# Kernel tuning notes

Measured on AMD Instinct MI355X. Metric: run time of the kernel, lower is better.

Reference implementation:

```python
import jax, jax.numpy as jnp
import numpy as np

B, T, DIM, H = 2, 2048, 1024, 16
HD = DIM // H  # head_dim = 64
ROPE_BASE = 10000.0


def setup_inputs() -> dict:
    key = jax.random.key(0)
    k1, k2, k3, k4 = jax.random.split(key, 4)
    s = 1.0 / np.sqrt(DIM)
    return {
        "x": jax.random.normal(k1, (B, T, DIM), dtype=jnp.float32),
        "Wqkv": jax.random.normal(k2, (DIM, 3 * DIM), dtype=jnp.float32) * s,
        "Wout": jax.random.normal(k3, (DIM, DIM), dtype=jnp.float32) * s,
        "bout": jax.random.normal(k4, (DIM,), dtype=jnp.float32) * 0.01,
    }


def _rotate_half(x):
    # interleaved rotation: (x0,x1,x2,x3,...) -> (-x1,x0,-x3,x2,...)
    x1 = x[..., ::2]
    x2 = x[..., 1::2]
    return jnp.stack((-x2, x1), axis=-1).reshape(x.shape)


def _rope_cos_sin(seq_len, dtype):
    inv_freq = 1.0 / (ROPE_BASE ** (jnp.arange(0, HD, 2, dtype=jnp.float32) / HD))
    t = jnp.arange(seq_len, dtype=jnp.float32)
    freqs = t[:, None] * inv_freq[None, :]          # [T, HD/2]
    emb = jnp.concatenate((freqs, freqs), axis=-1)  # [T, HD] (cat layout, as in source)
    return jnp.cos(emb).astype(dtype), jnp.sin(emb).astype(dtype)


def reference(x, Wqkv, Wout, bout):
    b, t, _ = x.shape
    qkv = x @ Wqkv                                  # [B, T, 3*DIM]
    q, k, v = jnp.split(qkv, 3, axis=-1)
    # b t (h d) -> b h t d
    reshape = lambda z: z.reshape(b, t, H, HD).transpose(0, 2, 1, 3)
    q, k, v = reshape(q), reshape(k), reshape(v)
    cos, sin = _rope_cos_sin(t, x.dtype)            # [T, HD]
    q = q * cos + _rotate_half(q) * sin
    k = k * cos + _rotate_half(k) * sin
    scale = HD ** -0.5
    scores = jnp.einsum("bhqd,bhkd->bhqk", q, k) * scale
    attn = jax.nn.softmax(scores, axis=-1)
    out = jnp.einsum("bhqk,bhkd->bhqd", attn, v)    # [B, H, T, HD]
    out = out.transpose(0, 2, 1, 3).reshape(b, t, DIM)
    return out @ Wout + bout
```

## Files before the change

kernel.cpp:

```cpp
#include <hip/hip_runtime.h>
#include <math.h>


typedef unsigned short u16;
typedef __attribute__((ext_vector_type(8))) short short8;
typedef __attribute__((ext_vector_type(4))) short short4v;
typedef __attribute__((ext_vector_type(4))) float f32x4;
typedef __attribute__((ext_vector_type(16))) float f32x16;

#define T_SEQ 2048

#if __has_builtin(__builtin_amdgcn_exp2f)
#define EXP2(x) __builtin_amdgcn_exp2f(x)
#else
#define EXP2(x) exp2f(x)
#endif

__device__ __forceinline__ float b2f(u16 u) {
    union { unsigned int i; float f; } x; x.i = ((unsigned int)u) << 16; return x.f;
}
__device__ __forceinline__ u16 f2b(float f) {
    union { float f; unsigned int i; } x; x.f = f;
    return (u16)((x.i + 0x7FFFu + ((x.i >> 16) & 1u)) >> 16);
}
__device__ __forceinline__ void gl_lds16(const u16* g, u16* l) {
    __builtin_amdgcn_global_load_lds(
        (const __attribute__((address_space(1))) unsigned int*)g,
        (__attribute__((address_space(3))) unsigned int*)l, 16, 0, 0);
}
__device__ __forceinline__ short4v pack4(float a, float b, float c, float d) {
    union { float f; unsigned int u; } xa, xb, xc, xd;
    xa.f = a; xb.f = b; xc.f = c; xd.f = d;
    union { unsigned int u2[2]; short4v s; } r;
    r.u2[0] = (xa.u >> 16) | (xb.u & 0xffff0000u);
    r.u2[1] = (xc.u >> 16) | (xd.u & 0xffff0000u);
    return r.s;
}

__global__ __launch_bounds__(256) void setup_kernel(
    const float* __restrict__ x, const float* __restrict__ Wqkv,
    const float* __restrict__ Wout, u16* __restrict__ xb,
    u16* __restrict__ WqkvT, u16* __restrict__ WoutT,
    float* __restrict__ costab, float* __restrict__ sintab)
{
    const int bid = blockIdx.x;
    const int tid = threadIdx.x;

    if (bid < 4096) {
        int i = (bid * 256 + tid) * 4;
        float4 v = *(const float4*)(x + i);
        ushort4 w;
        w.x = f2b(v.x); w.y = f2b(v.y); w.z = f2b(v.z); w.w = f2b(v.w);
        *(ushort4*)(xb + i) = w;
        return;
    }
    if (bid < 8192) {
        const float* in; u16* out; int R, Cn, bx, by;
        if (bid < 7168) { in = Wqkv; out = WqkvT; R = 1024; Cn = 3072;
                          int id = bid - 4096; bx = id % 96; by = id / 96; }
        else            { in = Wout; out = WoutT; R = 1024; Cn = 1024;
                          int id = bid - 7168; bx = id & 31; by = id >> 5; }
        __shared__ u16 tile[32][33];
        const int tx = tid & 31, ty = tid >> 5;
        const int r0 = by * 32, c0 = bx * 32;
#pragma unroll
        for (int rr = ty; rr < 32; rr += 8)
            tile[tx][rr] = f2b(in[(size_t)(r0 + rr) * Cn + c0 + tx]);
        __syncthreads();
#pragma unroll
        for (int rr = ty; rr < 32; rr += 8)
            out[(size_t)(c0 + rr) * R + r0 + tx] = tile[rr][tx];
        return;
    }
    {
        int idx = (bid - 8192) * 256 + tid;
        int t = idx >> 6, d = idx & 63;
        const float nl32 = -0.28782313662425576f;
        float f = __expf((float)(d & 31) * nl32);
        float s, c;
        __sincosf((float)t * f, &s, &c);
        costab[idx] = c; sintab[idx] = s;
    }
}

template<int OBF>
__global__ __launch_bounds__(256) void gemm_bt_mfma(
    const u16* __restrict__ A, const u16* __restrict__ Bt,
    void* __restrict__ Cv, const float* __restrict__ bias,
    int M, int N, int K)
{
    __shared__ u16 As[128 * 32];
    __shared__ u16 Bs[128 * 32];

    const int tid = threadIdx.x;
    const int wave = tid >> 6, lane = tid & 63;
    const int col = lane & 15, quad = lane >> 4;
    const int wm = (wave & 1) * 64, wn = (wave >> 1) * 64;
    const int m0 = blockIdx.y * 128, n0 = blockIdx.x * 128;

    f32x4 acc[4][4];
#pragma unroll
    for (int i = 0; i < 4; ++i)
#pragma unroll
        for (int j = 0; j < 4; ++j) acc[i][j] = f32x4{0.f, 0.f, 0.f, 0.f};

    const int c1 = tid, c2 = tid + 256;
    const u16* a1 = A + (size_t)(m0 + (c1 >> 2)) * K + (c1 & 3) * 8;
    const u16* a2 = A + (size_t)(m0 + (c2 >> 2)) * K + (c2 & 3) * 8;
    const u16* b1 = Bt + (size_t)(n0 + (c1 >> 2)) * K + (c1 & 3) * 8;
    const u16* b2 = Bt + (size_t)(n0 + (c2 >> 2)) * K + (c2 & 3) * 8;
    u16* la1 = As + c1 * 8; u16* la2 = As + c2 * 8;
    u16* lb1 = Bs + c1 * 8; u16* lb2 = Bs + c2 * 8;

    for (int k0 = 0; k0 < K; k0 += 32) {
        __syncthreads();
        gl_lds16(a1 + k0, la1);
        gl_lds16(a2 + k0, la2);
        gl_lds16(b1 + k0, lb1);
        gl_lds16(b2 + k0, lb2);
        __syncthreads();

        short8 af[4], bfr[4];
#pragma unroll
        for (int i = 0; i < 4; ++i) {
            af[i]  = *(const short8*)&As[(wm + i * 16 + col) * 32 + quad * 8];
            bfr[i] = *(const short8*)&Bs[(wn + i * 16 + col) * 32 + quad * 8];
        }
#pragma unroll
        for (int i = 0; i < 4; ++i)
#pragma unroll
            for (int j = 0; j < 4; ++j)
                acc[i][j] = __builtin_amdgcn_mfma_f32_16x16x32_bf16(
                    af[i], bfr[j], acc[i][j], 0, 0, 0);
    }

#pragma unroll
    for (int j = 0; j < 4; ++j) {
        int n = n0 + wn + j * 16 + col;
        float bv = bias ? bias[n] : 0.f;
#pragma unroll
        for (int i = 0; i < 4; ++i) {
            int mbase = m0 + wm + i * 16 + quad * 4;
#pragma unroll
            for (int r = 0; r < 4; ++r) {
                if (OBF) ((u16*)Cv)[(size_t)(mbase + r) * N + n] = f2b(acc[i][j][r] + bv);
                else     ((float*)Cv)[(size_t)(mbase + r) * N + n] = acc[i][j][r] + bv;
            }
        }
    }
}

__global__ __launch_bounds__(256) void prep_kernel(
    const u16* __restrict__ qkvb, const float* __restrict__ costab,
    const float* __restrict__ sintab, u16* __restrict__ Qb,
    u16* __restrict__ Kb, u16* __restrict__ Vimg)
{
    __shared__ u16 Vls[64][72];

    const int tid = threadIdx.x;
    const int bh = blockIdx.y;
    const int t0 = blockIdx.x * 64;
    const int b = bh >> 4, h = bh & 15;
    const int t_loc = tid >> 2;
    const int d0 = (tid & 3) * 16;

    const int t = t0 + t_loc;
    const u16* qp = qkvb + ((size_t)(b * T_SEQ + t)) * 3072 + h * 64 + d0;

    float ct[16], st[16];
    {
        const float* cp = costab + (size_t)t * 64 + d0;
        const float* sp = sintab + (size_t)t * 64 + d0;
#pragma unroll
        for (int j = 0; j < 16; j += 4) {
            *(float4*)&ct[j] = *(const float4*)(cp + j);
            *(float4*)&st[j] = *(const float4*)(sp + j);
        }
    }

#pragma unroll
    for (int part = 0; part < 2; ++part) {
        const float sc = part ? 1.f : 0.18033688011112042f;
        const u16* src = qp + part * 1024;
        u16* dst = (part ? Kb : Qb) + ((size_t)(bh * T_SEQ + t)) * 64 + d0;
        short8 v0 = *(const short8*)(src);
        short8 v1 = *(const short8*)(src + 8);
        float f[16];
#pragma unroll
        for (int j = 0; j < 8; ++j) { f[j] = b2f((u16)v0[j]); f[8 + j] = b2f((u16)v1[j]); }
        u16 o[16];
#pragma unroll
        for (int i = 0; i < 8; ++i) {
            float e = f[2 * i], od = f[2 * i + 1];
            o[2 * i]     = f2b((e * ct[2 * i]      - od * st[2 * i]) * sc);
            o[2 * i + 1] = f2b((od * ct[2 * i + 1] + e  * st[2 * i + 1]) * sc);
        }
        *(short8*)(dst)     = *(short8*)&o[0];
        *(short8*)(dst + 8) = *(short8*)&o[8];
    }

    {
        const u16* src = qp + 2048;
        *(short8*)&Vls[t_loc][d0]     = *(const short8*)(src);
        *(short8*)&Vls[t_loc][d0 + 8] = *(const short8*)(src + 8);
    }
    __syncthreads();
    {
        const int dt    = tid >> 7;
        const int g     = (tid >> 5) & 3;
        const int hi2   = (tid >> 4) & 1;
        const int dpair = tid & 15;
        const int kl0 = g * 8 + hi2 * 4;
        const int d0v = dt * 32 + 2 * dpair;
        const int kt_base = blockIdx.x * 2;
#pragma unroll
        for (int ktl = 0; ktl < 2; ++ktl) {
            u16 o[8];
#pragma unroll
            for (int j = 0; j < 4; ++j) {
                o[j]     = Vls[ktl * 32 + kl0 + j][d0v];
                o[4 + j] = Vls[ktl * 32 + kl0 + j][d0v + 1];
            }
            u16* dst = Vimg + ((size_t)(bh * 64 + kt_base + ktl)) * 2048 + tid * 8;
            *(short8*)dst = *(short8*)&o[0];
        }
    }
}

__global__ __launch_bounds__(256) void attn32_kernel(
    const u16* __restrict__ Qb, const u16* __restrict__ Kb,
    const u16* __restrict__ Vimg, float* __restrict__ po, float* __restrict__ pl)
{
    __shared__ u16 Kbuf[2][2048];
    __shared__ u16 Vbuf[2][2048];

    const int tid = threadIdx.x;
    const int wave = tid >> 6, lane = tid & 63;
    const int qcol = lane & 31;
    const int hi = lane >> 5;

    const int bid = blockIdx.x;
    const int bh = bid >> 5;
    const int seg = (bid >> 4) & 1;
    const int qblk = bid & 15;
    const int qrow0 = qblk * 128 + wave * 32;

    short8 qa[4];
    {
        const u16* qp = Qb + ((size_t)(bh * T_SEQ + qrow0 + qcol)) * 64 + hi * 8;
#pragma unroll
        for (int c = 0; c < 4; ++c) qa[c] = *(const short8*)(qp + c * 16);
    }

    f32x16 O0, O1;
#pragma unroll
    for (int i = 0; i < 16; ++i) { O0[i] = 0.f; O1[i] = 0.f; }
    float Lacc = 0.f;

    const u16* kg_ptr = Kb + ((size_t)bh * T_SEQ + qcol) * 64 + wave * 16 + hi * 8;
    const u16* vg_ptr = Vimg + ((size_t)bh * 64) * 2048 + tid * 8;

    const int kt0 = seg * 32;
    for (int r = 0; r < 16; ++r) {
        const int kt = kt0 + r * 2;
        __syncthreads();
        gl_lds16(kg_ptr + (size_t)kt * 2048,       &Kbuf[0][tid * 8]);
        gl_lds16(kg_ptr + (size_t)(kt + 1) * 2048, &Kbuf[1][tid * 8]);
        gl_lds16(vg_ptr + (size_t)kt * 2048,       &Vbuf[0][tid * 8]);
        gl_lds16(vg_ptr + (size_t)(kt + 1) * 2048, &Vbuf[1][tid * 8]);
        __syncthreads();

#pragma unroll
        for (int half = 0; half < 2; ++half) {
            short8 kf[4];
#pragma unroll
            for (int f = 0; f < 4; ++f)
                kf[f] = *(const short8*)&Kbuf[half][(f * 64 + lane) * 8];

            f32x16 sT;
#pragma unroll
            for (int ii = 0; ii < 16; ++ii) sT[ii] = 0.f;
#pragma unroll
            for (int c = 0; c < 4; ++c)
                sT = __builtin_amdgcn_mfma_f32_32x32x16_bf16(kf[c], qa[c], sT, 0, 0, 0);

            float pe[16];
#pragma unroll
            for (int ii = 0; ii < 16; ++ii) pe[ii] = EXP2(sT[ii]);
            short4v pb[4];
#pragma unroll
            for (int g = 0; g < 4; ++g) {
                pb[g] = pack4(pe[4 * g + 0], pe[4 * g + 1],
                              pe[4 * g + 2], pe[4 * g + 3]);
                Lacc += (pe[4 * g + 0] + pe[4 * g + 1]) +
                        (pe[4 * g + 2] + pe[4 * g + 3]);
            }

#pragma unroll
            for (int g = 0; g < 4; ++g) {
                short4v va0 = *(const short4v*)&Vbuf[half][g * 256 + lane * 4];
                short4v va1 = *(const short4v*)&Vbuf[half][1024 + g * 256 + lane * 4];
                O0 = __builtin_amdgcn_mfma_f32_32x32x8bf16_1k(va0, pb[g], O0, 0, 0, 0);
                O1 = __builtin_amdgcn_mfma_f32_32x32x8bf16_1k(va1, pb[g], O1, 0, 0, 0);
            }
        }
    }

    float Lq = Lacc + __shfl(Lacc, lane ^ 32);

    const size_t prow = ((size_t)(seg * 32 + bh)) * T_SEQ + qrow0 + qcol;
    float* op = po + prow * 64;
#pragma unroll
    for (int g2 = 0; g2 < 4; ++g2) {
        int dd = g2 * 8 + hi * 4;
        *(float4*)(op + dd)      = make_float4(O0[4 * g2 + 0], O0[4 * g2 + 1],
                                               O0[4 * g2 + 2], O0[4 * g2 + 3]);
        *(float4*)(op + 32 + dd) = make_float4(O1[4 * g2 + 0], O1[4 * g2 + 1],
                                               O1[4 * g2 + 2], O1[4 * g2 + 3]);
    }
    if (hi == 0) pl[prow] = Lq;
}

__global__ __launch_bounds__(256) void attn_combine_kernel(
    const float* __restrict__ po, const float* __restrict__ pl,
    u16* __restrict__ aob)
{
    const int idx = blockIdx.x * 256 + (int)threadIdx.x;
    const int row = idx >> 4;
    const int d4 = idx & 15;

    float4 o0 = *(const float4*)(po + (size_t)row * 64 + d4 * 4);
    float4 o1 = *(const float4*)(po + ((size_t)row + 65536) * 64 + d4 * 4);
    float L = pl[row] + pl[row + 65536];
    float inv = 1.f / L;

    const int bh = row >> 11, t = row & 2047;
    const int b = bh >> 4, h = bh & 15;
    ushort4 w;
    w.x = f2b((o0.x + o1.x) * inv);
    w.y = f2b((o0.y + o1.y) * inv);
    w.z = f2b((o0.z + o1.z) * inv);
    w.w = f2b((o0.w + o1.w) * inv);
    *(ushort4*)(aob + ((size_t)(b * T_SEQ + t)) * 1024 + h * 64 + d4 * 4) = w;
}

extern "C" void kernel_launch(void* const* d_in, const int* in_sizes, int n_in,
                              void* d_out, int out_size, void* d_ws, size_t ws_size,
                              hipStream_t stream)
{
    const float* x    = (const float*)d_in[0];
    const float* Wqkv = (const float*)d_in[1];
    const float* Wout = (const float*)d_in[2];
    const float* bout = (const float*)d_in[3];
    float* out = (float*)d_out;

    char* w = (char*)d_ws;
    u16* qkvb    = (u16*)(w);
    u16* xb      = (u16*)(w + 25165824);
    u16* WqkvT   = (u16*)(w + 33554432);
    u16* WoutT   = (u16*)(w + 39845888);
    u16* aob     = (u16*)(w + 41943040);
    u16* Qb      = (u16*)(w + 50331648);
    u16* Kb      = (u16*)(w + 58720256);
    u16* Vimg    = (u16*)(w + 67108864);
    float* ctab  = (float*)(w + 75497472);
    float* stab  = (float*)(w + 76021760);
    float* po    = (float*)(w);
    float* pl    = (float*)(w + 33554432);

    dim3 blk(256);
    setup_kernel<<<dim3(8704), blk, 0, stream>>>(x, Wqkv, Wout, xb, WqkvT, WoutT, ctab, stab);
    gemm_bt_mfma<1><<<dim3(24, 32), blk, 0, stream>>>(xb, WqkvT, qkvb, nullptr, 4096, 3072, 1024);
    prep_kernel<<<dim3(32, 32), blk, 0, stream>>>(qkvb, ctab, stab, Qb, Kb, Vimg);
    attn32_kernel<<<dim3(1024), blk, 0, stream>>>(Qb, Kb, Vimg, po, pl);
    attn_combine_kernel<<<dim3(4096), blk, 0, stream>>>(po, pl, aob);
    gemm_bt_mfma<0><<<dim3(8, 32), blk, 0, stream>>>(aob, WoutT, out, bout, 4096, 1024, 1024);
}
```

Baseline: 219.8 us.

## Double-buffer K/V tiles in LDS and prefetch next tile during attention compute

The attention kernel now keeps two LDS buffers for K and V. Before the loop it loads the first tile, and inside each iteration it moves the current tile's K and V fragments into registers and then issues async loads for the next tile. This lets global-to-LDS traffic overlap with the MFMA and exp work, and it cuts the loop from two barriers per step to one. It also adds a launch-bounds occupancy hint. In exchange it doubles the LDS footprint and raises register pressure from holding both halves' fragments at once.

```diff
diff --git a/kernel.cpp b/kernel.cpp
--- a/kernel.cpp
+++ b/kernel.cpp
@@ -227,12 +227,12 @@
     }
 }
 
-__global__ __launch_bounds__(256) void attn32_kernel(
+__global__ __launch_bounds__(256, 3) void attn32_kernel(
     const u16* __restrict__ Qb, const u16* __restrict__ Kb,
     const u16* __restrict__ Vimg, float* __restrict__ po, float* __restrict__ pl)
 {
-    __shared__ u16 Kbuf[2][2048];
-    __shared__ u16 Vbuf[2][2048];
+    __shared__ u16 Kbuf[2][2][2048];
+    __shared__ u16 Vbuf[2][2][2048];
 
     const int tid = threadIdx.x;
     const int wave = tid >> 6, lane = tid & 63;
@@ -261,28 +261,46 @@
     const u16* vg_ptr = Vimg + ((size_t)bh * 64) * 2048 + tid * 8;
 
     const int kt0 = seg * 32;
+
+    gl_lds16(kg_ptr + (size_t)kt0 * 2048,       &Kbuf[0][0][tid * 8]);
+    gl_lds16(kg_ptr + (size_t)(kt0 + 1) * 2048, &Kbuf[0][1][tid * 8]);
+    gl_lds16(vg_ptr + (size_t)kt0 * 2048,       &Vbuf[0][0][tid * 8]);
+    gl_lds16(vg_ptr + (size_t)(kt0 + 1) * 2048, &Vbuf[0][1][tid * 8]);
+    __syncthreads();
+
     for (int r = 0; r < 16; ++r) {
-        const int kt = kt0 + r * 2;
-        __syncthreads();
-        gl_lds16(kg_ptr + (size_t)kt * 2048,       &Kbuf[0][tid * 8]);
-        gl_lds16(kg_ptr + (size_t)(kt + 1) * 2048, &Kbuf[1][tid * 8]);
-        gl_lds16(vg_ptr + (size_t)kt * 2048,       &Vbuf[0][tid * 8]);
-        gl_lds16(vg_ptr + (size_t)(kt + 1) * 2048, &Vbuf[1][tid * 8]);
-        __syncthreads();
-
+        const int cur = r & 1;
+
+        short8 kf[2][4];
+        short4v vv[2][8];
 #pragma unroll
         for (int half = 0; half < 2; ++half) {
-            short8 kf[4];
 #pragma unroll
             for (int f = 0; f < 4; ++f)
-                kf[f] = *(const short8*)&Kbuf[half][(f * 64 + lane) * 8];
-
+                kf[half][f] = *(const short8*)&Kbuf[cur][half][(f * 64 + lane) * 8];
+#pragma unroll
+            for (int g = 0; g < 4; ++g) {
+                vv[half][2 * g]     = *(const short4v*)&Vbuf[cur][half][g * 256 + lane * 4];
+                vv[half][2 * g + 1] = *(const short4v*)&Vbuf[cur][half][1024 + g * 256 + lane * 4];
+            }
+        }
+
+        if (r < 15) {
+            const int kt = kt0 + (r + 1) * 2;
+            gl_lds16(kg_ptr + (size_t)kt * 2048,       &Kbuf[cur ^ 1][0][tid * 8]);
+            gl_lds16(kg_ptr + (size_t)(kt + 1) * 2048, &Kbuf[cur ^ 1][1][tid * 8]);
+            gl_lds16(vg_ptr + (size_t)kt * 2048,       &Vbuf[cur ^ 1][0][tid * 8]);
+            gl_lds16(vg_ptr + (size_t)(kt + 1) * 2048, &Vbuf[cur ^ 1][1][tid * 8]);
+        }
+
+#pragma unroll
+        for (int half = 0; half < 2; ++half) {
             f32x16 sT;
 #pragma unroll
             for (int ii = 0; ii < 16; ++ii) sT[ii] = 0.f;
 #pragma unroll
             for (int c = 0; c < 4; ++c)
-                sT = __builtin_amdgcn_mfma_f32_32x32x16_bf16(kf[c], qa[c], sT, 0, 0, 0);
+                sT = __builtin_amdgcn_mfma_f32_32x32x16_bf16(kf[half][c], qa[c], sT, 0, 0, 0);
 
             float pe[16];
 #pragma unroll
@@ -298,12 +316,12 @@
 
 #pragma unroll
             for (int g = 0; g < 4; ++g) {
-                short4v va0 = *(const short4v*)&Vbuf[half][g * 256 + lane * 4];
-                short4v va1 = *(const short4v*)&Vbuf[half][1024 + g * 256 + lane * 4];
-                O0 = __builtin_amdgcn_mfma_f32_32x32x8bf16_1k(va0, pb[g], O0, 0, 0, 0);
-                O1 = __builtin_amdgcn_mfma_f32_32x32x8bf16_1k(va1, pb[g], O1, 0, 0, 0);
-            }
-        }
+                O0 = __builtin_amdgcn_mfma_f32_32x32x8bf16_1k(vv[half][2 * g],     pb[g], O0, 0, 0, 0);
+                O1 = __builtin_amdgcn_mfma_f32_32x32x8bf16_1k(vv[half][2 * g + 1], pb[g], O1, 0, 0, 0);
+            }
+        }
+
+        __syncthreads();
     }
 
     float Lq = Lacc + __shfl(Lacc, lane ^ 32);
```

New measurement: 214.2 us. -2.5%, faster.

## Triple-buffer K/V tiles with async prefetch, XCD-aware block remap, and MFMA priority

Applied to the files above, without the earlier changes.

The attention kernel's K/V loading changes from synchronous double-tile loads, bracketed by two barriers per iteration, to a three-stage ring buffer. Each iteration prefetches the tile two steps ahead and waits with vmcnt counters, so there is a single barrier per key tile. Blocks are remapped so consecutive hardware block IDs, which are spread across XCDs, map to contiguous (bh, seg, qblk) work, aiming for better L2 reuse of K/V. The change also raises wave priority around MFMA sections and sets launch bounds to 4 blocks per CU; the extra shared memory buffer could limit occupancy.

```diff
diff --git a/kernel.cpp b/kernel.cpp
--- a/kernel.cpp
+++ b/kernel.cpp
@@ -227,12 +227,12 @@
     }
 }
 
-__global__ __launch_bounds__(256) void attn32_kernel(
+__global__ __launch_bounds__(256, 4) void attn32_kernel(
     const u16* __restrict__ Qb, const u16* __restrict__ Kb,
     const u16* __restrict__ Vimg, float* __restrict__ po, float* __restrict__ pl)
 {
-    __shared__ u16 Kbuf[2][2048];
-    __shared__ u16 Vbuf[2][2048];
+    __shared__ u16 Kbuf[3][2048];
+    __shared__ u16 Vbuf[3][2048];
 
     const int tid = threadIdx.x;
     const int wave = tid >> 6, lane = tid & 63;
@@ -240,9 +240,10 @@
     const int hi = lane >> 5;
 
     const int bid = blockIdx.x;
-    const int bh = bid >> 5;
-    const int seg = (bid >> 4) & 1;
-    const int qblk = bid & 15;
+    const int lbid = (bid & 7) * 128 + (bid >> 3);
+    const int bh = lbid >> 5;
+    const int seg = (lbid >> 4) & 1;
+    const int qblk = lbid & 15;
     const int qrow0 = qblk * 128 + wave * 32;
 
     short8 qa[4];
@@ -261,50 +262,69 @@
     const u16* vg_ptr = Vimg + ((size_t)bh * 64) * 2048 + tid * 8;
 
     const int kt0 = seg * 32;
-    for (int r = 0; r < 16; ++r) {
-        const int kt = kt0 + r * 2;
-        __syncthreads();
-        gl_lds16(kg_ptr + (size_t)kt * 2048,       &Kbuf[0][tid * 8]);
-        gl_lds16(kg_ptr + (size_t)(kt + 1) * 2048, &Kbuf[1][tid * 8]);
-        gl_lds16(vg_ptr + (size_t)kt * 2048,       &Vbuf[0][tid * 8]);
-        gl_lds16(vg_ptr + (size_t)(kt + 1) * 2048, &Vbuf[1][tid * 8]);
-        __syncthreads();
-
-#pragma unroll
-        for (int half = 0; half < 2; ++half) {
-            short8 kf[4];
-#pragma unroll
-            for (int f = 0; f < 4; ++f)
-                kf[f] = *(const short8*)&Kbuf[half][(f * 64 + lane) * 8];
-
-            f32x16 sT;
-#pragma unroll
-            for (int ii = 0; ii < 16; ++ii) sT[ii] = 0.f;
-#pragma unroll
-            for (int c = 0; c < 4; ++c)
-                sT = __builtin_amdgcn_mfma_f32_32x32x16_bf16(kf[c], qa[c], sT, 0, 0, 0);
-
-            float pe[16];
-#pragma unroll
-            for (int ii = 0; ii < 16; ++ii) pe[ii] = EXP2(sT[ii]);
-            short4v pb[4];
-#pragma unroll
-            for (int g = 0; g < 4; ++g) {
-                pb[g] = pack4(pe[4 * g + 0], pe[4 * g + 1],
-                              pe[4 * g + 2], pe[4 * g + 3]);
-                Lacc += (pe[4 * g + 0] + pe[4 * g + 1]) +
-                        (pe[4 * g + 2] + pe[4 * g + 3]);
-            }
-
-#pragma unroll
-            for (int g = 0; g < 4; ++g) {
-                short4v va0 = *(const short4v*)&Vbuf[half][g * 256 + lane * 4];
-                short4v va1 = *(const short4v*)&Vbuf[half][1024 + g * 256 + lane * 4];
-                O0 = __builtin_amdgcn_mfma_f32_32x32x8bf16_1k(va0, pb[g], O0, 0, 0, 0);
-                O1 = __builtin_amdgcn_mfma_f32_32x32x8bf16_1k(va1, pb[g], O1, 0, 0, 0);
-            }
-        }
-    }
+
+#define STAGE(p, rr) do {                                                     \
+        gl_lds16(kg_ptr + (size_t)(kt0 + (rr)) * 2048, &Kbuf[p][tid * 8]);    \
+        gl_lds16(vg_ptr + (size_t)(kt0 + (rr)) * 2048, &Vbuf[p][tid * 8]);    \
+    } while (0)
+
+    STAGE(0, 0);
+    STAGE(1, 1);
+
+    int cur = 0, prv = 2;
+    for (int r = 0; r < 32; ++r) {
+        if (r < 31) asm volatile("s_waitcnt vmcnt(2)" ::: "memory");
+        else        asm volatile("s_waitcnt vmcnt(0)" ::: "memory");
+        __builtin_amdgcn_s_barrier();
+        asm volatile("" ::: "memory");
+        __builtin_amdgcn_sched_barrier(0);
+
+        short8 kf[4];
+        short4v vv[8];
+#pragma unroll
+        for (int f = 0; f < 4; ++f)
+            kf[f] = *(const short8*)&Kbuf[cur][(f * 64 + lane) * 8];
+#pragma unroll
+        for (int g = 0; g < 4; ++g) {
+            vv[2 * g]     = *(const short4v*)&Vbuf[cur][g * 256 + lane * 4];
+            vv[2 * g + 1] = *(const short4v*)&Vbuf[cur][1024 + g * 256 + lane * 4];
+        }
+
+        if (r < 30) STAGE(prv, r + 2);
+
+        f32x16 sT;
+#pragma unroll
+        for (int ii = 0; ii < 16; ++ii) sT[ii] = 0.f;
+        __builtin_amdgcn_s_setprio(1);
+#pragma unroll
+        for (int c = 0; c < 4; ++c)
+            sT = __builtin_amdgcn_mfma_f32_32x32x16_bf16(kf[c], qa[c], sT, 0, 0, 0);
+        __builtin_amdgcn_s_setprio(0);
+
+        float pe[16];
+#pragma unroll
+        for (int ii = 0; ii < 16; ++ii) pe[ii] = EXP2(sT[ii]);
+        short4v pb[4];
+#pragma unroll
+        for (int g = 0; g < 4; ++g) {
+            pb[g] = pack4(pe[4 * g + 0], pe[4 * g + 1],
+                          pe[4 * g + 2], pe[4 * g + 3]);
+            Lacc += (pe[4 * g + 0] + pe[4 * g + 1]) +
+                    (pe[4 * g + 2] + pe[4 * g + 3]);
+        }
+
+        __builtin_amdgcn_s_setprio(1);
+#pragma unroll
+        for (int g = 0; g < 4; ++g) {
+            O0 = __builtin_amdgcn_mfma_f32_32x32x8bf16_1k(vv[2 * g],     pb[g], O0, 0, 0, 0);
+            O1 = __builtin_amdgcn_mfma_f32_32x32x8bf16_1k(vv[2 * g + 1], pb[g], O1, 0, 0, 0);
+        }
+        __builtin_amdgcn_s_setprio(0);
+
+        prv = cur;
+        cur = (cur == 2) ? 0 : cur + 1;
+    }
+#undef STAGE
 
     float Lq = Lacc + __shfl(Lacc, lane ^ 32);
 
```

After: 211.9 us. 3.6% less time.
